# Optimization experiments

Hardware: AMD Instinct MI355X
Metric: run time of the kernel (lower is better)

The kernel has to match this reference:

```python
import jax, jax.numpy as jnp
import numpy as np

N = 100000   # nodes
E = 1600000  # edges
IN = 128     # input feature dim
C = 64       # per-layer output dim (filters)
H = 2        # attention heads
EPS = 1e-5   # batchnorm eps


def setup_inputs() -> dict:
    key = jax.random.key(0)
    ks = jax.random.split(key, 32)
    rn = lambda k, s, sc=0.05: jax.random.normal(k, s, jnp.float32) * sc
    inp = {
        "x": jax.random.normal(ks[0], (N, IN), jnp.float32),
        "edge_index": jax.random.randint(ks[1], (2, E), 0, N, jnp.int32),
        # GATConv layer 0 (IN -> C, H heads, concat=False)
        "W0": rn(ks[2], (IN, H * C)), "as0": rn(ks[3], (H, C)), "ad0": rn(ks[4], (H, C)), "b0": jnp.zeros((C,), jnp.float32),
        "skip0": rn(ks[5], (IN, C)),  # Linear(IN->C, bias=False); layers 1,2 skips are Identity
        "g0": jnp.ones((C,), jnp.float32), "be0": jnp.zeros((C,), jnp.float32),
        # GATConv layer 1 (C -> C)
        "W1": rn(ks[6], (C, H * C)), "as1": rn(ks[7], (H, C)), "ad1": rn(ks[8], (H, C)), "b1": jnp.zeros((C,), jnp.float32),
        "g1": jnp.ones((C,), jnp.float32), "be1": jnp.zeros((C,), jnp.float32),
        # GATConv layer 2 (C -> C)
        "W2": rn(ks[9], (C, H * C)), "as2": rn(ks[10], (H, C)), "ad2": rn(ks[11], (H, C)), "b2": jnp.zeros((C,), jnp.float32),
        "g2": jnp.ones((C,), jnp.float32), "be2": jnp.zeros((C,), jnp.float32),
        # JK projection for input (IN -> C, with bias); other projections are Identity
        "projW": rn(ks[12], (IN, C)), "projb": jnp.zeros((C,), jnp.float32),
    }
    return inp


def _gat(x, edge_index, W, a_src, a_dst, b):
    # PyG GATConv, concat=False: mean over heads, bias added after mean.
    h = (x @ W).reshape(-1, H, C)                 # [N, H, C]
    src, dst = edge_index[0], edge_index[1]
    e_src = jnp.sum(h * a_src, axis=-1)           # [N, H]
    e_dst = jnp.sum(h * a_dst, axis=-1)           # [N, H]
    e = jax.nn.leaky_relu(e_src[src] + e_dst[dst], 0.2)  # [E, H]
    m = jax.ops.segment_max(e, dst, num_segments=N)      # neighbor softmax (stable)
    w = jnp.exp(e - m[dst])
    denom = jax.ops.segment_sum(w, dst, num_segments=N)
    alpha = w / (denom[dst] + 1e-16)              # [E, H]
    out = jax.ops.segment_sum(alpha[:, :, None] * h[src], dst, num_segments=N)  # [N, H, C]
    return out.mean(axis=1) + b


def _bn(x, g, b):
    # BatchNorm1d, training-mode batch statistics (deterministic reference)
    mu = x.mean(axis=0)
    var = x.var(axis=0)
    return (x - mu) * jax.lax.rsqrt(var + EPS) * g + b


def reference(x, edge_index, W0, as0, ad0, b0, skip0, g0, be0,
              W1, as1, ad1, b1, g1, be1,
              W2, as2, ad2, b2, g2, be2,
              projW, projb):
    lrelu = lambda v: jax.nn.leaky_relu(v, 0.01)  # nn.LeakyReLU default
    jk0 = x @ projW + projb                       # proj_lyrs[0]
    # layer 0: GAT + projected skip, BN, (dropout=identity in eval), LeakyReLU
    h1 = _gat(x, edge_index, W0, as0, ad0, b0) + x @ skip0
    h1 = lrelu(_bn(h1, g0, be0))
    # layer 1: identity skip
    h2 = _gat(h1, edge_index, W1, as1, ad1, b1) + h1
    h2 = lrelu(_bn(h2, g1, be1))
    # layer 2: identity skip
    h3 = _gat(h2, edge_index, W2, as2, ad2, b2) + h2
    h3 = lrelu(_bn(h3, g2, be2))
    # jumping knowledge, mode='max': elementwise max over [input_proj, h1, h2, h3]
    return jnp.max(jnp.stack([jk0, h1, h2, h3], axis=0), axis=0)
```

## Files before the change

### kernel.cpp

```cpp
#include <hip/hip_runtime.h>

#define NN 100000
#define NE 1600000

constexpr int NBUC = 196;
constexpr int BIN_CHUNK = 4096;
constexpr int NB_BIN = (NE + BIN_CHUNK - 1) / BIN_CHUNK;
constexpr int NPART = 512;

typedef __attribute__((ext_vector_type(8))) short s16x8;
typedef __attribute__((ext_vector_type(4))) float f32x4;
typedef __attribute__((ext_vector_type(2))) float f32x2;

template <int M>
struct IC {
    static constexpr int value = M;
};

__device__ inline unsigned short f2bf(float f) {
    unsigned int u = __float_as_uint(f);
    return (unsigned short)((u + 0x7fffu + ((u >> 16) & 1u)) >> 16);
}
__device__ inline float bf_lo(unsigned int pk) { return __uint_as_float(pk << 16); }
__device__ inline float bf_hi(unsigned int pk) { return __uint_as_float(pk & 0xffff0000u); }
__device__ inline float h2f(unsigned int u) {
    _Float16 h;
    unsigned short s = (unsigned short)u;
    __builtin_memcpy(&h, &s, 2);
    return (float)h;
}

__global__ void zero_u32(unsigned int* p, int n) {
    int i = blockIdx.x * blockDim.x + threadIdx.x;
    if (i < n) p[i] = 0u;
}

__global__ __launch_bounds__(256) void bucket_count(const int* __restrict__ dst,
                                                    int* __restrict__ bcount) {
    __shared__ int hist[NBUC];
    int t = threadIdx.x;
    for (int b = t; b < NBUC; b += 256) hist[b] = 0;
    __syncthreads();
    int beg = blockIdx.x * BIN_CHUNK;
    int end = min(beg + BIN_CHUNK, NE);
    for (int i = beg + t; i < end; i += 256) atomicAdd(&hist[dst[i] >> 9], 1);
    __syncthreads();
    for (int b = t; b < NBUC; b += 256)
        if (hist[b]) atomicAdd(&bcount[b], hist[b]);
}

__global__ void bucket_scan(const int* __restrict__ bcount, int* __restrict__ bbase,
                            int* __restrict__ bucket_cursor, int* __restrict__ offsets) {
    if (threadIdx.x == 0) {
        int run = 0;
        for (int b = 0; b < NBUC; ++b) {
            bbase[b] = run;
            bucket_cursor[b] = run;
            run += bcount[b];
        }
        bbase[NBUC] = NE;
        offsets[NN] = NE;
    }
}

__global__ __launch_bounds__(256) void bin_edges(const int* __restrict__ src,
                                                 const int* __restrict__ dst,
                                                 int* __restrict__ bucket_cursor,
                                                 unsigned int* __restrict__ binned) {
    __shared__ int hist[NBUC];
    __shared__ int base[NBUC];
    int t = threadIdx.x;
    for (int b = t; b < NBUC; b += 256) hist[b] = 0;
    __syncthreads();
    int beg = blockIdx.x * BIN_CHUNK;
    int end = min(beg + BIN_CHUNK, NE);
    for (int i = beg + t; i < end; i += 256) atomicAdd(&hist[dst[i] >> 9], 1);
    __syncthreads();
    for (int b = t; b < NBUC; b += 256) {
        base[b] = hist[b] ? atomicAdd(&bucket_cursor[b], hist[b]) : 0;
        hist[b] = 0;
    }
    __syncthreads();
    for (int i = beg + t; i < end; i += 256) {
        int d = dst[i];
        int bk = d >> 9;
        int loc = atomicAdd(&hist[bk], 1);
        binned[base[bk] + loc] = ((unsigned)(d & 511) << 17) | (unsigned)src[i];
    }
}

__global__ __launch_bounds__(256) void bucket_sort(const unsigned int* __restrict__ binned,
                                                   const int* __restrict__ bbase,
                                                   int* __restrict__ offsets,
                                                   int* __restrict__ csr_src,
                                                   int* __restrict__ csr_dst) {
    __shared__ int deg[512];
    __shared__ int loc[512];
    __shared__ int s2[256];
    int t = threadIdx.x;
    int b = blockIdx.x;
    int beg = bbase[b], end = bbase[b + 1];
    int nbase = b << 9;
    deg[t] = 0;
    deg[t + 256] = 0;
    __syncthreads();
    for (int i = beg + t; i < end; i += 256) atomicAdd(&deg[binned[i] >> 17], 1);
    __syncthreads();
    int pairsum = deg[2 * t] + deg[2 * t + 1];
    s2[t] = pairsum;
    __syncthreads();
    for (int off = 1; off < 256; off <<= 1) {
        int v = (t >= off) ? s2[t - off] : 0;
        __syncthreads();
        s2[t] += v;
        __syncthreads();
    }
    int ex = s2[t] - pairsum;
    loc[2 * t] = ex;
    loc[2 * t + 1] = ex + deg[2 * t];
    __syncthreads();
    for (int i = t; i < 512; i += 256) {
        int node = nbase + i;
        if (node < NN) offsets[node] = beg + loc[i];
    }
    __syncthreads();
    for (int i = beg + t; i < end; i += 256) {
        unsigned int v = binned[i];
        int dl = v >> 17;
        int pos = atomicAdd(&loc[dl], 1);
        csr_src[beg + pos] = (int)(v & 0x1FFFFu);
        csr_dst[beg + pos] = nbase + dl;
    }
}

__global__ void prep_weights(const float* __restrict__ W0, const float* __restrict__ skip0,
                             const float* __restrict__ projW, const float* __restrict__ W1,
                             const float* __restrict__ W2,
                             const float* __restrict__ as0, const float* __restrict__ ad0,
                             const float* __restrict__ as1, const float* __restrict__ ad1,
                             const float* __restrict__ as2, const float* __restrict__ ad2,
                             unsigned short* __restrict__ Wtcat,
                             unsigned short* __restrict__ Wt1,
                             unsigned short* __restrict__ Wt2) {
    int i = blockIdx.x * 256 + threadIdx.x;
    if (i < 16384) {
        int oc = i >> 7, k = i & 127;
        Wtcat[oc * 128 + k] = f2bf(W0[k * 128 + oc]);
    } else if (i < 32768) {
        int j = i - 16384;
        int oc = j >> 7, k = j & 127;
        float v = (oc < 64) ? skip0[k * 64 + oc] : projW[k * 64 + (oc - 64)];
        Wtcat[132 * 128 + oc * 128 + k] = f2bf(v);
    } else if (i < 40960) {
        int j = i - 32768, oc = j >> 6, k = j & 63;
        Wt1[oc * 64 + k] = f2bf(W1[k * 128 + oc]);
    } else if (i < 49152) {
        int j = i - 40960, oc = j >> 6, k = j & 63;
        Wt2[oc * 64 + k] = f2bf(W2[k * 128 + oc]);
    } else if (i < 50688) {
        int e = i - 49152;
        if (e < 512) {
            int k = e >> 2, sc = e & 3, head = sc & 1;
            const float* av = (sc < 2 ? as0 : ad0) + head * 64;
            const float* wr = W0 + k * 128 + head * 64;
            float s = 0.f;
            for (int c = 0; c < 64; ++c) s += wr[c] * av[c];
            Wtcat[(128 + sc) * 128 + k] = f2bf(s);
        } else if (e < 1024) {
            int j = e - 512, k = j >> 2, sc = j & 3;
            Wtcat[132 * 128 + (128 + sc) * 128 + k] = 0;
        } else if (e < 1280) {
            int j = e - 1024, k = j >> 2, sc = j & 3, head = sc & 1;
            const float* av = (sc < 2 ? as1 : ad1) + head * 64;
            const float* wr = W1 + k * 128 + head * 64;
            float s = 0.f;
            for (int c = 0; c < 64; ++c) s += wr[c] * av[c];
            Wt1[(128 + sc) * 64 + k] = f2bf(s);
        } else {
            int j = e - 1280, k = j >> 2, sc = j & 3, head = sc & 1;
            const float* av = (sc < 2 ? as2 : ad2) + head * 64;
            const float* wr = W2 + k * 128 + head * 64;
            float s = 0.f;
            for (int c = 0; c < 64; ++c) s += wr[c] * av[c];
            Wt2[(128 + sc) * 64 + k] = f2bf(s);
        }
    }
}

template <int K, bool L0, bool XFORM>
__global__ __launch_bounds__(256, 4) void gemm_mfma(
    const void* __restrict__ Xv, const unsigned short* __restrict__ Wt,
    unsigned int* __restrict__ Hq32, _Float16* __restrict__ skipx,
    _Float16* __restrict__ jkproj, const float* __restrict__ projb,
    const float* __restrict__ bnsc,
    unsigned int* __restrict__ e_srcpk, unsigned int* __restrict__ e_dstpk) {
    constexpr int KP = K + 8;
    constexpr int NC = 132;
    __shared__ unsigned short Bs[NC * KP];
    int t = threadIdx.x;
    int tile = L0 ? blockIdx.x : 0;
    int rbase = (L0 ? blockIdx.y : blockIdx.x) * 64;
    const unsigned short* Wtg = Wt + (size_t)tile * NC * K;

    for (int i = t; i < NC * (K / 8); i += 256) {
        int oc = i / (K / 8);
        int k8 = (i % (K / 8)) * 8;
        uint4 v = *(const uint4*)&Wtg[(size_t)oc * K + k8];
        *(uint4*)&Bs[oc * KP + k8] = v;
    }

    int lane = t & 63, wv = t >> 6;
    int lr = lane & 15, quad = lane >> 4;
    int arow = wv * 16 + lr;
    int grow = rbase + arow;
    bool rowok = grow < NN;

    s16x8 afrag[K / 32];
#pragma unroll
    for (int ks = 0; ks < K / 32; ++ks) {
        int kq = ks * 32 + quad * 8;
        float v[8];
        if (rowok) {
            if constexpr (!XFORM) {
                const float* Xf = (const float*)Xv;
                float4 p0 = *(const float4*)&Xf[(size_t)grow * K + kq];
                float4 p1 = *(const float4*)&Xf[(size_t)grow * K + kq + 4];
                v[0] = p0.x; v[1] = p0.y; v[2] = p0.z; v[3] = p0.w;
                v[4] = p1.x; v[5] = p1.y; v[6] = p1.z; v[7] = p1.w;
            } else {
                const _Float16* Xh = (const _Float16*)Xv;
                uint4 rw = *(const uint4*)&Xh[(size_t)grow * K + kq];
                unsigned rr[4] = {rw.x, rw.y, rw.z, rw.w};
#pragma unroll
                for (int q = 0; q < 4; ++q) {
                    v[2 * q] = h2f(rr[q]);
                    v[2 * q + 1] = h2f(rr[q] >> 16);
                }
#pragma unroll
                for (int c = 0; c < 8; ++c) {
                    float val = v[c] * bnsc[kq + c] + bnsc[64 + kq + c];
                    v[c] = val >= 0.f ? val : 0.01f * val;
                }
            }
        } else {
#pragma unroll
            for (int c = 0; c < 8; ++c) v[c] = 0.f;
        }
        unsigned short* ap = (unsigned short*)&afrag[ks];
#pragma unroll
        for (int c = 0; c < 8; ++c) ap[c] = f2bf(v[c]);
    }
    __syncthreads();

    f32x4 acc[8];
    f32x4 acc8 = (f32x4)(0.f);
#pragma unroll
    for (int c = 0; c < 8; ++c) acc[c] = (f32x4)(0.f);
#pragma unroll
    for (int ks = 0; ks < K / 32; ++ks) {
        s16x8 a = afrag[ks];
        int k0 = ks * 32;
#pragma unroll
        for (int ct = 0; ct < 8; ++ct) {
            s16x8 b = *(const s16x8*)&Bs[(ct * 16 + lr) * KP + k0 + quad * 8];
            acc[ct] = __builtin_amdgcn_mfma_f32_16x16x32_bf16(a, b, acc[ct], 0, 0, 0);
        }
        s16x8 b9 = *(const s16x8*)&Bs[(128 + (lr & 3)) * KP + k0 + quad * 8];
        acc8 = __builtin_amdgcn_mfma_f32_16x16x32_bf16(a, b9, acc8, 0, 0, 0);
    }

    bool hblock = (!L0) || (tile == 0);
#pragma unroll
    for (int reg = 0; reg < 4; ++reg) {
        int row = rbase + wv * 16 + quad * 4 + reg;
        if (hblock) {
            if (row < NN) {
#pragma unroll
                for (int ct = 0; ct < 4; ++ct) {
                    int pk = __builtin_amdgcn_cvt_pk_fp8_f32(acc[ct][reg], acc[ct + 4][reg],
                                                             0, false);
                    int pn = __shfl_xor(pk, 1, 64);
                    if (!(lr & 1))
                        Hq32[(size_t)row * 32 + ct * 8 + (lr >> 1)] =
                            (unsigned int)((pk & 0xFFFF) | (pn << 16));
                }
            }
            float own = acc8[reg];
            float par = __shfl_xor(own, 1, 64);
            if (row < NN) {
                unsigned int pkv = (unsigned)f2bf(own) | ((unsigned)f2bf(par) << 16);
                if (lr == 0) e_srcpk[row] = pkv;
                else if (lr == 2) e_dstpk[row] = pkv;
            }
        } else if (row < NN) {
#pragma unroll
            for (int ct = 0; ct < 4; ++ct)
                skipx[(size_t)row * 64 + ct * 16 + lr] = (_Float16)acc[ct][reg];
#pragma unroll
            for (int ct = 4; ct < 8; ++ct) {
                int c = (ct - 4) * 16 + lr;
                jkproj[(size_t)row * 64 + c] = (_Float16)(acc[ct][reg] + projb[c]);
            }
        }
    }
}

__global__ void edge_w(const int* __restrict__ csr_src, const int* __restrict__ csr_dst,
                       const unsigned int* __restrict__ e_srcpk,
                       const unsigned int* __restrict__ e_dstpk,
                       uint2* __restrict__ erec) {
    int i = blockIdx.x * blockDim.x + threadIdx.x;
    if (i >= NE) return;
    int s = csr_src[i];
    unsigned int q = e_srcpk[s];
    unsigned int r = e_dstpk[csr_dst[i]];
    float a0 = bf_lo(q) + bf_lo(r);
    float a1 = bf_hi(q) + bf_hi(r);
    a0 = a0 >= 0.f ? a0 : 0.2f * a0;
    a1 = a1 >= 0.f ? a1 : 0.2f * a1;
    unsigned int w = (unsigned int)f2bf(__expf(a0)) | ((unsigned int)f2bf(__expf(a1)) << 16);
    erec[i] = make_uint2((unsigned)s, w);
}

__global__ __launch_bounds__(256) void aggregate(
    const int* __restrict__ offsets, const uint2* __restrict__ erec,
    const unsigned int* __restrict__ Hq32, const _Float16* __restrict__ skipsrc,
    const float* __restrict__ bnsc, const float* __restrict__ bias,
    _Float16* __restrict__ hraw) {
    int wave = threadIdx.x >> 6;
    int lane = threadIdx.x & 63;
    int n = blockIdx.x * 4 + wave;
    if (n >= NN) return;
    const unsigned char* __restrict__ Hq8 = (const unsigned char*)Hq32;
    int beg = __builtin_amdgcn_readfirstlane(offsets[n]);
    int end = __builtin_amdgcn_readfirstlane(offsets[n + 1]);
    int voff = lane * 2;

    float sv = (float)skipsrc[(size_t)n * 64 + lane];
    float bi = bias[lane];
    float bsc = 0.f, bsh = 0.f;
    if (bnsc) {
        bsc = bnsc[lane];
        bsh = bnsc[64 + lane];
    }

    float a0 = 0.f, a1 = 0.f, den0 = 0.f, den1 = 0.f;
    int j = beg;

    auto batch = [&](auto Mc) {
        constexpr int M = decltype(Mc)::value;
        uint2 ee[M];
#pragma unroll
        for (int u = 0; u < M; ++u) ee[u] = erec[j + u];
        int ss[M];
        unsigned ww[M];
#pragma unroll
        for (int u = 0; u < M; ++u) {
            ss[u] = __builtin_amdgcn_readfirstlane((int)ee[u].x);
            ww[u] = (unsigned)__builtin_amdgcn_readfirstlane((int)ee[u].y);
        }
        unsigned short uu[M];
#pragma unroll
        for (int u = 0; u < M; ++u)
            uu[u] = *(const unsigned short*)(Hq8 + (size_t)ss[u] * 128 + voff);
#pragma unroll
        for (int u = 0; u < M; ++u) {
            float w0 = bf_lo(ww[u]), w1 = bf_hi(ww[u]);
            f32x2 hv = __builtin_amdgcn_cvt_pk_f32_fp8((int)uu[u], false);
            den0 += w0;
            den1 += w1;
            a0 += w0 * hv[0];
            a1 += w1 * hv[1];
        }
        j += M;
    };

    while (j + 16 <= end) batch(IC<16>{});
    if (j + 8 <= end) batch(IC<8>{});
    if (j + 4 <= end) batch(IC<4>{});
    if (j + 2 <= end) batch(IC<2>{});
    if (j < end) batch(IC<1>{});

    if (bnsc) {
        sv = sv * bsc + bsh;
        sv = sv >= 0.f ? sv : 0.01f * sv;
    }
    float id0 = 1.f / (den0 + 1e-16f), id1 = 1.f / (den1 + 1e-16f);
    float o = 0.5f * (a0 * id0 + a1 * id1) + bi + sv;
    hraw[(size_t)n * 64 + lane] = (_Float16)o;
}

__global__ __launch_bounds__(256) void bn_stats(const _Float16* __restrict__ x,
                                                float* __restrict__ part) {
    __shared__ float lsum[64], lsum2[64];
    int t = threadIdx.x;
    int c8 = t & 7, q = t >> 3;
    int cbase = c8 * 8;
    float s[8], s2[8];
#pragma unroll
    for (int k = 0; k < 8; ++k) s[k] = s2[k] = 0.f;
    for (int r = blockIdx.x * 32 + q; r < NN; r += NPART * 32) {
        uint4 v = *(const uint4*)&x[(size_t)r * 64 + cbase];
        unsigned rr[4] = {v.x, v.y, v.z, v.w};
#pragma unroll
        for (int k = 0; k < 4; ++k) {
            float f0 = h2f(rr[k]);
            float f1 = h2f(rr[k] >> 16);
            s[2 * k] += f0;
            s2[2 * k] += f0 * f0;
            s[2 * k + 1] += f1;
            s2[2 * k + 1] += f1 * f1;
        }
    }
    if (t < 64) {
        lsum[t] = 0.f;
        lsum2[t] = 0.f;
    }
    __syncthreads();
#pragma unroll
    for (int k = 0; k < 8; ++k) {
        atomicAdd(&lsum[cbase + k], s[k]);
        atomicAdd(&lsum2[cbase + k], s2[k]);
    }
    __syncthreads();
    if (t < 128)
        part[(size_t)blockIdx.x * 128 + t] = (t < 64) ? lsum[t] : lsum2[t - 64];
}

__global__ __launch_bounds__(1024) void bn_final(const float* __restrict__ part,
                                                 const float* __restrict__ g,
                                                 const float* __restrict__ be,
                                                 float* __restrict__ sc_sh) {
    __shared__ float tot[8][128];
    int t = threadIdx.x;
    int c = t & 127, gh = t >> 7;
    float s = 0.f;
    for (int b = gh * (NPART / 8); b < (gh + 1) * (NPART / 8); ++b)
        s += part[(size_t)b * 128 + c];
    tot[gh][c] = s;
    __syncthreads();
    if (t < 128) {
        float v = tot[0][t];
#pragma unroll
        for (int k = 1; k < 8; ++k) v += tot[k][t];
        tot[0][t] = v;
    }
    __syncthreads();
    if (t < 64) {
        float mu = tot[0][t] / (float)NN;
        float var = tot[0][64 + t] / (float)NN - mu * mu;
        float sc = g[t] * rsqrtf(var + 1e-5f);
        sc_sh[t] = sc;
        sc_sh[64 + t] = be[t] - mu * sc;
    }
}

__global__ void final_out(const _Float16* __restrict__ jkproj, const _Float16* __restrict__ hA,
                          const _Float16* __restrict__ hB, const _Float16* __restrict__ hC,
                          const float* __restrict__ bnAll, float* __restrict__ out) {
    int i = blockIdx.x * blockDim.x + threadIdx.x;
    if (i < NN * 64) {
        int c = i & 63;
        float v0 = (float)hA[i] * bnAll[c] + bnAll[64 + c];
        float v1 = (float)hB[i] * bnAll[128 + c] + bnAll[192 + c];
        float v2 = (float)hC[i] * bnAll[256 + c] + bnAll[320 + c];
        v0 = v0 >= 0.f ? v0 : 0.01f * v0;
        v1 = v1 >= 0.f ? v1 : 0.01f * v1;
        v2 = v2 >= 0.f ? v2 : 0.01f * v2;
        out[i] = fmaxf(fmaxf((float)jkproj[i], v0), fmaxf(v1, v2));
    }
}

extern "C" void kernel_launch(void* const* d_in, const int* in_sizes, int n_in,
                              void* d_out, int out_size, void* d_ws, size_t ws_size,
                              hipStream_t stream) {
    const float* x = (const float*)d_in[0];
    const int* ei = (const int*)d_in[1];
    const int* e_src_idx = ei;
    const int* e_dst_idx = ei + NE;
    const float* W0 = (const float*)d_in[2];
    const float* as0 = (const float*)d_in[3];
    const float* ad0 = (const float*)d_in[4];
    const float* b0 = (const float*)d_in[5];
    const float* skip0 = (const float*)d_in[6];
    const float* g0 = (const float*)d_in[7];
    const float* be0 = (const float*)d_in[8];
    const float* W1 = (const float*)d_in[9];
    const float* as1 = (const float*)d_in[10];
    const float* ad1 = (const float*)d_in[11];
    const float* b1 = (const float*)d_in[12];
    const float* g1 = (const float*)d_in[13];
    const float* be1 = (const float*)d_in[14];
    const float* W2 = (const float*)d_in[15];
    const float* as2 = (const float*)d_in[16];
    const float* ad2 = (const float*)d_in[17];
    const float* b2 = (const float*)d_in[18];
    const float* g2 = (const float*)d_in[19];
    const float* be2 = (const float*)d_in[20];
    const float* projW = (const float*)d_in[21];
    const float* projb = (const float*)d_in[22];
    float* out = (float*)d_out;

    char* p = (char*)d_ws;
    auto alloc = [&](size_t bytes) {
        char* r = p;
        p += (bytes + 255) & ~(size_t)255;
        return r;
    };
    int* zbuf = (int*)alloc((size_t)196 * 4);
    int* bcount = zbuf;
    int* bbase = (int*)alloc((size_t)(NBUC + 1) * 4);
    int* bucket_cursor = (int*)alloc((size_t)NBUC * 4);
    int* offsets = (int*)alloc((size_t)(NN + 1) * 4);
    int* csr_src = (int*)alloc((size_t)NE * 4);
    int* csr_dst = (int*)alloc((size_t)NE * 4);
    uint2* erec = (uint2*)alloc((size_t)NE * 8);
    unsigned int* binned = (unsigned int*)alloc((size_t)NE * 4);
    unsigned int* h_q32 = (unsigned int*)alloc((size_t)NN * 32 * 4);
    unsigned int* e_srcpk = (unsigned int*)alloc((size_t)NN * 4);
    unsigned int* e_dstpk = (unsigned int*)alloc((size_t)NN * 4);
    _Float16* skipx = (_Float16*)alloc((size_t)NN * 64 * 2);
    _Float16* jkproj = (_Float16*)alloc((size_t)NN * 64 * 2);
    _Float16* hrawA = (_Float16*)alloc((size_t)NN * 64 * 2);
    _Float16* hrawB = (_Float16*)alloc((size_t)NN * 64 * 2);
    _Float16* hrawC = (_Float16*)alloc((size_t)NN * 64 * 2);
    unsigned short* Wtcat = (unsigned short*)alloc((size_t)2 * 132 * 128 * 2);
    unsigned short* Wt1 = (unsigned short*)alloc((size_t)132 * 64 * 2);
    unsigned short* Wt2 = (unsigned short*)alloc((size_t)132 * 64 * 2);
    float* bnscAll = (float*)alloc(3 * 128 * 4);
    float* part = (float*)alloc((size_t)NPART * 128 * 4);
    if ((size_t)(p - (char*)d_ws) > ws_size) return;

    zero_u32<<<1, 256, 0, stream>>>((unsigned int*)zbuf, 196);
    bucket_count<<<NB_BIN, 256, 0, stream>>>(e_dst_idx, bcount);
    bucket_scan<<<1, 64, 0, stream>>>(bcount, bbase, bucket_cursor, offsets);
    bin_edges<<<NB_BIN, 256, 0, stream>>>(e_src_idx, e_dst_idx, bucket_cursor, binned);
    bucket_sort<<<NBUC, 256, 0, stream>>>(binned, bbase, offsets, csr_src, csr_dst);
    prep_weights<<<198, 256, 0, stream>>>(W0, skip0, projW, W1, W2, as0, ad0, as1, ad1,
                                          as2, ad2, Wtcat, Wt1, Wt2);

    int gblocks = (NN + 63) / 64;
    int ablocks = (NN + 3) / 4;

    gemm_mfma<128, true, false><<<dim3(2, gblocks), 256, 0, stream>>>(
        x, Wtcat, h_q32, skipx, jkproj, projb, nullptr, e_srcpk, e_dstpk);
    edge_w<<<(NE + 255) / 256, 256, 0, stream>>>(csr_src, csr_dst, e_srcpk, e_dstpk, erec);
    aggregate<<<ablocks, 256, 0, stream>>>(offsets, erec, h_q32, skipx, nullptr, b0,
                                           hrawA);
    bn_stats<<<NPART, 256, 0, stream>>>(hrawA, part);
    bn_final<<<1, 1024, 0, stream>>>(part, g0, be0, bnscAll);

    gemm_mfma<64, false, true><<<dim3(gblocks, 1), 256, 0, stream>>>(
        hrawA, Wt1, h_q32, nullptr, nullptr, nullptr, bnscAll, e_srcpk, e_dstpk);
    edge_w<<<(NE + 255) / 256, 256, 0, stream>>>(csr_src, csr_dst, e_srcpk, e_dstpk, erec);
    aggregate<<<ablocks, 256, 0, stream>>>(offsets, erec, h_q32, hrawA, bnscAll, b1,
                                           hrawB);
    bn_stats<<<NPART, 256, 0, stream>>>(hrawB, part);
    bn_final<<<1, 1024, 0, stream>>>(part, g1, be1, bnscAll + 128);

    gemm_mfma<64, false, true><<<dim3(gblocks, 1), 256, 0, stream>>>(
        hrawB, Wt2, h_q32, nullptr, nullptr, nullptr, bnscAll + 128, e_srcpk, e_dstpk);
    edge_w<<<(NE + 255) / 256, 256, 0, stream>>>(csr_src, csr_dst, e_srcpk, e_dstpk, erec);
    aggregate<<<ablocks, 256, 0, stream>>>(offsets, erec, h_q32, hrawB, bnscAll + 128,
                                           b2, hrawC);
    bn_stats<<<NPART, 256, 0, stream>>>(hrawC, part);
    bn_final<<<1, 1024, 0, stream>>>(part, g2, be2, bnscAll + 256);

    final_out<<<(NN * 64 + 255) / 256, 256, 0, stream>>>(jkproj, hrawA, hrawB, hrawC,
                                                         bnscAll, out);
}
```

Before: 491.0 us.

## Use per-block bucket histograms with a scan and finer buckets for CSR build

Replaces the global atomic bucket cursors with per-block histograms written to a partition table, followed by a single-block column scan that gives each block deterministic bucket bases. This removes the zeroing kernel and the second counting pass in bin_edges. Buckets shrink from 512 to 128 nodes (782 buckets), so bucket_sort gets more blocks with smaller shared scans. final_out is also vectorised to process four channels per thread. The single-block scan serially walks 391 rows per column, which may add latency.

```diff
diff --git a/kernel.cpp b/kernel.cpp
--- a/kernel.cpp
+++ b/kernel.cpp
@@ -3,7 +3,7 @@
 #define NN 100000
 #define NE 1600000
 
-constexpr int NBUC = 196;
+constexpr int NBUC = 782;
 constexpr int BIN_CHUNK = 4096;
 constexpr int NB_BIN = (NE + BIN_CHUNK - 1) / BIN_CHUNK;
 constexpr int NPART = 512;
@@ -30,34 +30,49 @@
     return (float)h;
 }
 
-__global__ void zero_u32(unsigned int* p, int n) {
-    int i = blockIdx.x * blockDim.x + threadIdx.x;
-    if (i < n) p[i] = 0u;
-}
-
 __global__ __launch_bounds__(256) void bucket_count(const int* __restrict__ dst,
-                                                    int* __restrict__ bcount) {
+                                                    int* __restrict__ part) {
     __shared__ int hist[NBUC];
     int t = threadIdx.x;
     for (int b = t; b < NBUC; b += 256) hist[b] = 0;
     __syncthreads();
     int beg = blockIdx.x * BIN_CHUNK;
     int end = min(beg + BIN_CHUNK, NE);
-    for (int i = beg + t; i < end; i += 256) atomicAdd(&hist[dst[i] >> 9], 1);
-    __syncthreads();
-    for (int b = t; b < NBUC; b += 256)
-        if (hist[b]) atomicAdd(&bcount[b], hist[b]);
-}
-
-__global__ void bucket_scan(const int* __restrict__ bcount, int* __restrict__ bbase,
-                            int* __restrict__ bucket_cursor, int* __restrict__ offsets) {
-    if (threadIdx.x == 0) {
-        int run = 0;
-        for (int b = 0; b < NBUC; ++b) {
-            bbase[b] = run;
-            bucket_cursor[b] = run;
-            run += bcount[b];
-        }
+    for (int i = beg + t; i < end; i += 256) atomicAdd(&hist[dst[i] >> 7], 1);
+    __syncthreads();
+    for (int b = t; b < NBUC; b += 256) part[blockIdx.x * NBUC + b] = hist[b];
+}
+
+__global__ __launch_bounds__(1024) void csr_scan(int* __restrict__ part,
+                                                 int* __restrict__ bbase,
+                                                 int* __restrict__ offsets) {
+    __shared__ int tot[NBUC];
+    __shared__ int sc[1024];
+    int t = threadIdx.x;
+    int colsum = 0;
+    if (t < NBUC) {
+        for (int r = 0; r < NB_BIN; ++r) colsum += part[r * NBUC + t];
+        tot[t] = colsum;
+    }
+    sc[t] = (t < NBUC) ? colsum : 0;
+    __syncthreads();
+    for (int off = 1; off < 1024; off <<= 1) {
+        int v = (t >= off) ? sc[t - off] : 0;
+        __syncthreads();
+        sc[t] += v;
+        __syncthreads();
+    }
+    if (t < NBUC) {
+        int ex = sc[t] - tot[t];
+        bbase[t] = ex;
+        int run = ex;
+        for (int r = 0; r < NB_BIN; ++r) {
+            int tmp = part[r * NBUC + t];
+            part[r * NBUC + t] = run;
+            run += tmp;
+        }
+    }
+    if (t == 0) {
         bbase[NBUC] = NE;
         offsets[NN] = NE;
     }
@@ -65,27 +80,23 @@
 
 __global__ __launch_bounds__(256) void bin_edges(const int* __restrict__ src,
                                                  const int* __restrict__ dst,
-                                                 int* __restrict__ bucket_cursor,
+                                                 const int* __restrict__ part,
                                                  unsigned int* __restrict__ binned) {
+    __shared__ int base[NBUC];
     __shared__ int hist[NBUC];
-    __shared__ int base[NBUC];
-    int t = threadIdx.x;
-    for (int b = t; b < NBUC; b += 256) hist[b] = 0;
+    int t = threadIdx.x;
+    for (int b = t; b < NBUC; b += 256) {
+        base[b] = part[blockIdx.x * NBUC + b];
+        hist[b] = 0;
+    }
     __syncthreads();
     int beg = blockIdx.x * BIN_CHUNK;
     int end = min(beg + BIN_CHUNK, NE);
-    for (int i = beg + t; i < end; i += 256) atomicAdd(&hist[dst[i] >> 9], 1);
-    __syncthreads();
-    for (int b = t; b < NBUC; b += 256) {
-        base[b] = hist[b] ? atomicAdd(&bucket_cursor[b], hist[b]) : 0;
-        hist[b] = 0;
-    }
-    __syncthreads();
     for (int i = beg + t; i < end; i += 256) {
         int d = dst[i];
-        int bk = d >> 9;
+        int bk = d >> 7;
         int loc = atomicAdd(&hist[bk], 1);
-        binned[base[bk] + loc] = ((unsigned)(d & 511) << 17) | (unsigned)src[i];
+        binned[base[bk] + loc] = ((unsigned)(d & 127) << 17) | (unsigned)src[i];
     }
 }
 
@@ -94,34 +105,30 @@
                                                    int* __restrict__ offsets,
                                                    int* __restrict__ csr_src,
                                                    int* __restrict__ csr_dst) {
-    __shared__ int deg[512];
-    __shared__ int loc[512];
-    __shared__ int s2[256];
+    __shared__ int deg[128];
+    __shared__ int loc[128];
+    __shared__ int s2[128];
     int t = threadIdx.x;
     int b = blockIdx.x;
     int beg = bbase[b], end = bbase[b + 1];
-    int nbase = b << 9;
-    deg[t] = 0;
-    deg[t + 256] = 0;
+    int nbase = b << 7;
+    if (t < 128) deg[t] = 0;
     __syncthreads();
     for (int i = beg + t; i < end; i += 256) atomicAdd(&deg[binned[i] >> 17], 1);
     __syncthreads();
-    int pairsum = deg[2 * t] + deg[2 * t + 1];
-    s2[t] = pairsum;
-    __syncthreads();
-    for (int off = 1; off < 256; off <<= 1) {
-        int v = (t >= off) ? s2[t - off] : 0;
+    if (t < 128) s2[t] = deg[t];
+    __syncthreads();
+    for (int off = 1; off < 128; off <<= 1) {
+        int v = (t >= off && t < 128) ? s2[t - off] : 0;
         __syncthreads();
-        s2[t] += v;
+        if (t < 128) s2[t] += v;
         __syncthreads();
     }
-    int ex = s2[t] - pairsum;
-    loc[2 * t] = ex;
-    loc[2 * t + 1] = ex + deg[2 * t];
-    __syncthreads();
-    for (int i = t; i < 512; i += 256) {
-        int node = nbase + i;
-        if (node < NN) offsets[node] = beg + loc[i];
+    if (t < 128) {
+        int ex = s2[t] - deg[t];
+        loc[t] = ex;
+        int node = nbase + t;
+        if (node < NN) offsets[node] = beg + ex;
     }
     __syncthreads();
     for (int i = beg + t; i < end; i += 256) {
@@ -459,16 +466,30 @@
                           const _Float16* __restrict__ hB, const _Float16* __restrict__ hC,
                           const float* __restrict__ bnAll, float* __restrict__ out) {
     int i = blockIdx.x * blockDim.x + threadIdx.x;
-    if (i < NN * 64) {
-        int c = i & 63;
-        float v0 = (float)hA[i] * bnAll[c] + bnAll[64 + c];
-        float v1 = (float)hB[i] * bnAll[128 + c] + bnAll[192 + c];
-        float v2 = (float)hC[i] * bnAll[256 + c] + bnAll[320 + c];
+    if (i >= NN * 16) return;
+    int c0 = (i & 15) * 4;
+    uint2 vj = *(const uint2*)&jkproj[(size_t)i * 4];
+    uint2 va = *(const uint2*)&hA[(size_t)i * 4];
+    uint2 vb = *(const uint2*)&hB[(size_t)i * 4];
+    uint2 vc = *(const uint2*)&hC[(size_t)i * 4];
+    unsigned ja[2] = {vj.x, vj.y}, aa[2] = {va.x, va.y};
+    unsigned ba[2] = {vb.x, vb.y}, ca[2] = {vc.x, vc.y};
+    float4 o;
+    float* op = (float*)&o;
+#pragma unroll
+    for (int k = 0; k < 4; ++k) {
+        int c = c0 + k;
+        unsigned sh = (k & 1) * 16;
+        float fj = h2f(ja[k >> 1] >> sh);
+        float v0 = h2f(aa[k >> 1] >> sh) * bnAll[c] + bnAll[64 + c];
+        float v1 = h2f(ba[k >> 1] >> sh) * bnAll[128 + c] + bnAll[192 + c];
+        float v2 = h2f(ca[k >> 1] >> sh) * bnAll[256 + c] + bnAll[320 + c];
         v0 = v0 >= 0.f ? v0 : 0.01f * v0;
         v1 = v1 >= 0.f ? v1 : 0.01f * v1;
         v2 = v2 >= 0.f ? v2 : 0.01f * v2;
-        out[i] = fmaxf(fmaxf((float)jkproj[i], v0), fmaxf(v1, v2));
-    }
+        op[k] = fmaxf(fmaxf(fj, v0), fmaxf(v1, v2));
+    }
+    *(float4*)&out[(size_t)i * 4] = o;
 }
 
 extern "C" void kernel_launch(void* const* d_in, const int* in_sizes, int n_in,
@@ -507,10 +528,8 @@
         p += (bytes + 255) & ~(size_t)255;
         return r;
     };
-    int* zbuf = (int*)alloc((size_t)196 * 4);
-    int* bcount = zbuf;
+    int* partbins = (int*)alloc((size_t)NB_BIN * NBUC * 4);
     int* bbase = (int*)alloc((size_t)(NBUC + 1) * 4);
-    int* bucket_cursor = (int*)alloc((size_t)NBUC * 4);
     int* offsets = (int*)alloc((size_t)(NN + 1) * 4);
     int* csr_src = (int*)alloc((size_t)NE * 4);
     int* csr_dst = (int*)alloc((size_t)NE * 4);
@@ -531,10 +550,9 @@
     float* part = (float*)alloc((size_t)NPART * 128 * 4);
     if ((size_t)(p - (char*)d_ws) > ws_size) return;
 
-    zero_u32<<<1, 256, 0, stream>>>((unsigned int*)zbuf, 196);
-    bucket_count<<<NB_BIN, 256, 0, stream>>>(e_dst_idx, bcount);
-    bucket_scan<<<1, 64, 0, stream>>>(bcount, bbase, bucket_cursor, offsets);
-    bin_edges<<<NB_BIN, 256, 0, stream>>>(e_src_idx, e_dst_idx, bucket_cursor, binned);
+    bucket_count<<<NB_BIN, 256, 0, stream>>>(e_dst_idx, partbins);
+    csr_scan<<<1, 1024, 0, stream>>>(partbins, bbase, offsets);
+    bin_edges<<<NB_BIN, 256, 0, stream>>>(e_src_idx, e_dst_idx, partbins, binned);
     bucket_sort<<<NBUC, 256, 0, stream>>>(binned, bbase, offsets, csr_src, csr_dst);
     prep_weights<<<198, 256, 0, stream>>>(W0, skip0, projW, W1, W2, as0, ad0, as1, ad1,
                                           as2, ad2, Wtcat, Wt1, Wt2);
@@ -566,6 +584,6 @@
     bn_stats<<<NPART, 256, 0, stream>>>(hrawC, part);
     bn_final<<<1, 1024, 0, stream>>>(part, g2, be2, bnscAll + 256);
 
-    final_out<<<(NN * 64 + 255) / 256, 256, 0, stream>>>(jkproj, hrawA, hrawB, hrawC,
+    final_out<<<(NN * 16 + 255) / 256, 256, 0, stream>>>(jkproj, hrawA, hrawB, hrawC,
                                                          bnscAll, out);
 }
```

After: 512.8 us. +4.4%, slower.
